# Performance work log

Measured on AMD Instinct MI355X. Metric: run time of the kernel, lower is better.

## Reference

```python
import jax, jax.numpy as jnp
import numpy as np

IN_FEATURES = 256
N_HEADS = 4
N_HIDDEN = 128  # out_features, concat=False
SLOPE = 0.1
NEG_INF = -9e15


def setup_inputs() -> dict:
    key = jax.random.key(0)
    k1, k2, k3, k4 = jax.random.split(key, 4)
    N = 8192
    h = jax.random.normal(k1, (N, IN_FEATURES), dtype=jnp.float32)
    adj_mat = jax.random.randint(k2, (N, N), 0, 2, dtype=jnp.int32)
    # xavier_normal with gain=1.414
    std_W = 1.414 * (2.0 / (IN_FEATURES + N_HIDDEN * N_HEADS)) ** 0.5
    W = jax.random.normal(k3, (IN_FEATURES, N_HIDDEN * N_HEADS), dtype=jnp.float32) * std_W
    std_a = 1.414 * (2.0 / (2 * N_HIDDEN + 1)) ** 0.5
    a = jax.random.normal(k4, (N_HEADS, 2 * N_HIDDEN, 1), dtype=jnp.float32) * std_a
    return {"h": h, "adj_mat": adj_mat, "W": W, "a": a}


def reference(h, adj_mat, W, a):
    N = h.shape[0]
    # linear projection -> [H, N, d]
    ht = (h @ W).reshape(N, N_HEADS, N_HIDDEN).transpose(1, 0, 2)
    # dropout is identity (eval / p effectively 0), then LeakyReLU
    ht = jnp.where(ht >= 0, ht, SLOPE * ht)
    # additive attention scores: src[h,i] + tgt[h,j]
    src = jnp.einsum('hnd,hd->hn', ht, a[:, :N_HIDDEN, 0])  # [H, N]
    tgt = jnp.einsum('hnd,hd->hn', ht, a[:, N_HIDDEN:, 0])  # [H, N]
    e = src[:, :, None] + tgt[:, None, :]                   # [H, N, N]
    e = jnp.where(adj_mat[None, :, :] > 0, e, NEG_INF)
    attn = jax.nn.softmax(e, axis=-1)
    # weighted sum and mean over heads (concat=False)
    out = jnp.einsum('hnm,hmd->hnd', attn, ht).mean(axis=0)  # [N, d]
    return out
```

## Files before the change

### kernel.cpp

```cpp
#include <hip/hip_runtime.h>


typedef unsigned short u16;
typedef unsigned int u32;
using bf16x8 = __attribute__((ext_vector_type(8))) short;
using f32x4  = __attribute__((ext_vector_type(4))) float;

typedef const void __attribute__((address_space(1))) gas_void;
typedef void __attribute__((address_space(3))) las_void;
#define GLD16(g, l) __builtin_amdgcn_global_load_lds((gas_void*)(g), (las_void*)(l), 16, 0, 0)

__device__ __forceinline__ u16 f2bf(float f) {
  u32 u = __float_as_uint(f);
  return (u16)((u + 0x7FFFu + ((u >> 16) & 1u)) >> 16);
}
__device__ __forceinline__ float bf2f(u16 u) {
  return __uint_as_float(((u32)u) << 16);
}

__global__ void transpose_w(const float* __restrict__ W, float* __restrict__ Wt) {
  __shared__ float tile[32][33];
  int cb = blockIdx.x * 32, kb = blockIdx.y * 32;
  int tc = threadIdx.x & 31, tr = threadIdx.x >> 5;
  for (int p = 0; p < 32; p += 8)
    tile[tr + p][tc] = W[(size_t)(kb + tr + p) * 512 + cb + tc];
  __syncthreads();
  for (int p = 0; p < 32; p += 8)
    Wt[(size_t)(cb + tr + p) * 256 + kb + tc] = tile[tc][tr + p];
}

__global__ void ht_gemm(const float* __restrict__ h, const float* __restrict__ Wt,
                        u16* __restrict__ HT) {
  __shared__ __align__(16) u16 Abuf[128 * 40];
  __shared__ __align__(16) u16 Bbuf[128 * 40];
  int tid = threadIdx.x;
  int cb = blockIdx.x, rb = blockIdx.y;
  int r0 = rb * 128, c0 = cb * 128;
  int lane = tid & 63, wv = tid >> 6;
  int wr = wv >> 1, wc = wv & 1;
  int mrow = lane & 15, q = lane >> 4;
  int ch = tid & 7, m0 = tid >> 3;

  f32x4 acc[4][4];
#pragma unroll
  for (int i = 0; i < 4; i++)
#pragma unroll
    for (int j = 0; j < 4; j++) acc[i][j] = f32x4{0.f, 0.f, 0.f, 0.f};

  for (int kt = 0; kt < 256; kt += 32) {
    __syncthreads();
#pragma unroll
    for (int mp = 0; mp < 128; mp += 32) {
      int m = m0 + mp;
      float4 v = *(const float4*)(&h[(size_t)(r0 + m) * 256 + kt + ch * 4]);
      uint2 p;
      p.x = (u32)f2bf(v.x) | ((u32)f2bf(v.y) << 16);
      p.y = (u32)f2bf(v.z) | ((u32)f2bf(v.w) << 16);
      *(uint2*)(&Abuf[m * 40 + ch * 4]) = p;
      float4 u = *(const float4*)(&Wt[(size_t)(c0 + m) * 256 + kt + ch * 4]);
      uint2 r;
      r.x = (u32)f2bf(u.x) | ((u32)f2bf(u.y) << 16);
      r.y = (u32)f2bf(u.z) | ((u32)f2bf(u.w) << 16);
      *(uint2*)(&Bbuf[m * 40 + ch * 4]) = r;
    }
    __syncthreads();
    bf16x8 af[4], bfv[4];
#pragma unroll
    for (int i = 0; i < 4; i++)
      af[i] = *(const bf16x8*)(&Abuf[(wr * 64 + i * 16 + mrow) * 40 + q * 8]);
#pragma unroll
    for (int j = 0; j < 4; j++)
      bfv[j] = *(const bf16x8*)(&Bbuf[(wc * 64 + j * 16 + mrow) * 40 + q * 8]);
#pragma unroll
    for (int i = 0; i < 4; i++)
#pragma unroll
      for (int j = 0; j < 4; j++)
        acc[i][j] = __builtin_amdgcn_mfma_f32_16x16x32_bf16(af[i], bfv[j], acc[i][j], 0, 0, 0);
  }
#pragma unroll
  for (int i = 0; i < 4; i++)
#pragma unroll
    for (int j = 0; j < 4; j++)
#pragma unroll
      for (int r = 0; r < 4; r++) {
        int gi = r0 + wr * 64 + i * 16 + q * 4 + r;
        int gc = c0 + wc * 64 + j * 16 + mrow;
        float v = acc[i][j][r];
        v = v >= 0.f ? v : 0.1f * v;
        HT[(size_t)gi * 512 + gc] = f2bf(v);
      }
}

__global__ void build_yt(const u16* __restrict__ HT, const float* __restrict__ a,
                         u16* __restrict__ Yt) {
  __shared__ u16 sht[64][528];
  __shared__ float swv[64 * 4];
  __shared__ float sa[512];
  int t = threadIdx.x;
  int j0 = blockIdx.x * 64;
  for (int i = t; i < 512; i += 256) {
    int g = i >> 7, d = i & 127;
    sa[i] = a[g * 256 + 128 + d];
  }
#pragma unroll
  for (int p = 0; p < 16; ++p) {
    int el = t + 256 * p;
    int row = el >> 6, col8 = el & 63;
    *(uint4*)(&sht[row][col8 * 8]) = *(const uint4*)(&HT[(size_t)(j0 + row) * 512 + col8 * 8]);
  }
  __syncthreads();
  {
    int jl = t >> 2, g = t & 3;
    float acc = 0.f;
#pragma unroll
    for (int d8 = 0; d8 < 16; ++d8) {
      bf16x8 v = *(const bf16x8*)(&sht[jl][g * 128 + d8 * 8]);
#pragma unroll
      for (int u = 0; u < 8; ++u)
        acc += bf2f((u16)v[u]) * sa[g * 128 + d8 * 8 + u];
    }
    swv[jl * 4 + g] = __expf(acc);
  }
  __syncthreads();
  int oj = (t & 7) * 8, oc = t >> 3;
  for (int pass = 0; pass < 17; ++pass) {
    int c = pass * 32 + oc;
    if (c >= 528) break;
    u32 pk[4] = {0u, 0u, 0u, 0u};
    if (c < 512) {
      int g = c >> 7;
#pragma unroll
      for (int u = 0; u < 4; ++u) {
        int j = oj + 2 * u;
        float v0 = bf2f(sht[j][c]) * swv[j * 4 + g];
        float v1 = bf2f(sht[j + 1][c]) * swv[(j + 1) * 4 + g];
        pk[u] = (u32)f2bf(v0) | ((u32)f2bf(v1) << 16);
      }
    } else if (c < 516) {
      int g = c - 512;
#pragma unroll
      for (int u = 0; u < 4; ++u) {
        int j = oj + 2 * u;
        float v0 = swv[j * 4 + g];
        float v1 = swv[(j + 1) * 4 + g];
        pk[u] = (u32)f2bf(v0) | ((u32)f2bf(v1) << 16);
      }
    }
    *(uint4*)(&Yt[(size_t)c * 8192 + j0 + oj]) = make_uint4(pk[0], pk[1], pk[2], pk[3]);
  }
}

__global__ __launch_bounds__(256) void adj_gemm(const int* __restrict__ adj,
                                                const u16* __restrict__ Yt,
                                                float* __restrict__ C,
                                                float* __restrict__ S) {
  __shared__ __align__(16) u16 Abuf[128 * 32];
  __shared__ __align__(16) u16 Bbuf[128 * 32];
  __shared__ __align__(16) u16 Bden[16 * 32];
  int tid = threadIdx.x;
  int cb = blockIdx.x, rb = blockIdx.y, kh = blockIdx.z;
  int r0 = rb * 128, c0 = cb * 128, k0 = kh * 2048, kend = k0 + 2048;
  int lane = tid & 63, wv = tid >> 6;
  int wr = wv >> 1, wc = wv & 1;
  int mrow = lane & 15, q = lane >> 4;
  int arow = tid >> 2, aslot = tid & 3;
  int brow = lane >> 2, bq = lane & 3;
  int bo = bq ^ ((brow >> 1) & 3);
  bool do_den = (cb == 0) && (wc == 0);
  int s8 = (q ^ ((mrow >> 1) & 3)) * 8;

  f32x4 acc[4][4];
#pragma unroll
  for (int i = 0; i < 4; i++)
#pragma unroll
    for (int j = 0; j < 4; j++) acc[i][j] = f32x4{0.f, 0.f, 0.f, 0.f};
  f32x4 accD[4];
#pragma unroll
  for (int i = 0; i < 4; i++) accD[i] = f32x4{0.f, 0.f, 0.f, 0.f};

  for (int kt = k0; kt < kend; kt += 32) {
    __syncthreads();
#pragma unroll
    for (int p = 0; p < 2; ++p) {
      int m = p * 64 + arow;
      int o = aslot ^ ((m >> 1) & 3);
      const int* ap = &adj[(size_t)(r0 + m) * 8192 + kt + o * 8];
      int4 v0 = *(const int4*)(ap);
      int4 v1 = *(const int4*)(ap + 4);
      uint4 pk;
      pk.x = 16256u * ((u32)v0.x | ((u32)v0.y << 16));
      pk.y = 16256u * ((u32)v0.z | ((u32)v0.w << 16));
      pk.z = 16256u * ((u32)v1.x | ((u32)v1.y << 16));
      pk.w = 16256u * ((u32)v1.z | ((u32)v1.w << 16));
      *(uint4*)(&Abuf[m * 32 + aslot * 8]) = pk;
    }
#pragma unroll
    for (int p = 0; p < 2; ++p) {
      int g0 = (wv * 2 + p) * 16;
      GLD16(&Yt[(size_t)(c0 + g0 + brow) * 8192 + kt + bo * 8], &Bbuf[g0 * 32]);
    }
    if (cb == 0 && wv == 0)
      GLD16(&Yt[(size_t)(512 + brow) * 8192 + kt + bo * 8], Bden);
    __syncthreads();
    bf16x8 af[4], bfv[4];
#pragma unroll
    for (int i = 0; i < 4; i++)
      af[i] = *(const bf16x8*)(&Abuf[(wr * 64 + i * 16 + mrow) * 32 + s8]);
#pragma unroll
    for (int j = 0; j < 4; j++)
      bfv[j] = *(const bf16x8*)(&Bbuf[(wc * 64 + j * 16 + mrow) * 32 + s8]);
#pragma unroll
    for (int i = 0; i < 4; i++)
#pragma unroll
      for (int j = 0; j < 4; j++)
        acc[i][j] = __builtin_amdgcn_mfma_f32_16x16x32_bf16(af[i], bfv[j], acc[i][j], 0, 0, 0);
    if (do_den) {
      bf16x8 bd = *(const bf16x8*)(&Bden[mrow * 32 + s8]);
#pragma unroll
      for (int i = 0; i < 4; i++)
        accD[i] = __builtin_amdgcn_mfma_f32_16x16x32_bf16(af[i], bd, accD[i], 0, 0, 0);
    }
  }
  float* Ck = C + (size_t)kh * 8192 * 512;
#pragma unroll
  for (int i = 0; i < 4; i++)
#pragma unroll
    for (int j = 0; j < 4; j++)
#pragma unroll
      for (int r = 0; r < 4; r++) {
        int gi = r0 + wr * 64 + i * 16 + q * 4 + r;
        int gc = c0 + wc * 64 + j * 16 + mrow;
        Ck[(size_t)gi * 512 + gc] = acc[i][j][r];
      }
  if (do_den && mrow < 4) {
    float* Sk = S + (size_t)kh * 4 * 8192;
#pragma unroll
    for (int i = 0; i < 4; i++)
#pragma unroll
      for (int r = 0; r < 4; r++) {
        int gi = r0 + wr * 64 + i * 16 + q * 4 + r;
        Sk[(size_t)mrow * 8192 + gi] = accD[i][r];
      }
  }
}

__global__ void finalize_gat(const float* __restrict__ C, const float* __restrict__ S,
                             float* __restrict__ out) {
  int idx = blockIdx.x * 256 + threadIdx.x;
  int i = idx >> 7, d = idx & 127;
  float s = 0.f;
#pragma unroll
  for (int g = 0; g < 4; ++g) {
    float num = 0.f, den = 0.f;
#pragma unroll
    for (int kh = 0; kh < 4; ++kh) {
      num += C[(size_t)kh * 8192 * 512 + (size_t)i * 512 + g * 128 + d];
      den += S[(size_t)kh * 4 * 8192 + (size_t)g * 8192 + i];
    }
    s += num / den;
  }
  out[idx] = 0.25f * s;
}

extern "C" void kernel_launch(void* const* d_in, const int* in_sizes, int n_in,
                              void* d_out, int out_size, void* d_ws, size_t ws_size,
                              hipStream_t stream) {
  const float* h   = (const float*)d_in[0];
  const int*   adj = (const int*)d_in[1];
  const float* W   = (const float*)d_in[2];
  const float* a   = (const float*)d_in[3];
  float* out = (float*)d_out;
  char* ws = (char*)d_ws;
  float* Wt = (float*)(ws + 0);
  u16*   HT = (u16*)(ws + 524288);
  u16*   Yt = (u16*)(ws + 8912896);
  float* C  = (float*)(ws + 17563648);
  float* S  = (float*)(ws + 84672512);

  transpose_w<<<dim3(16, 8), 256, 0, stream>>>(W, Wt);
  ht_gemm<<<dim3(4, 64), 256, 0, stream>>>(h, Wt, HT);
  build_yt<<<dim3(128), 256, 0, stream>>>(HT, a, Yt);
  adj_gemm<<<dim3(4, 64, 4), 256, 0, stream>>>(adj, Yt, C, S);
  finalize_gat<<<dim3(4096), 256, 0, stream>>>(C, S, out);
}
```

Measured before the change: 560.2 us.

## Retile adjacency GEMM to 64x256 with K=64 steps and split denominator kernel

```diff
diff --git a/kernel.cpp b/kernel.cpp
--- a/kernel.cpp
+++ b/kernel.cpp
@@ -154,37 +154,35 @@
                                                 const u16* __restrict__ Yt,
                                                 float* __restrict__ C,
                                                 float* __restrict__ S) {
-  __shared__ __align__(16) u16 Abuf[128 * 32];
-  __shared__ __align__(16) u16 Bbuf[128 * 32];
-  __shared__ __align__(16) u16 Bden[16 * 32];
+  __shared__ __align__(16) u16 Abuf[64 * 64];
+  __shared__ __align__(16) u16 Bbuf[256 * 64];
+  __shared__ __align__(16) u16 Bden[16 * 64];
   int tid = threadIdx.x;
   int cb = blockIdx.x, rb = blockIdx.y, kh = blockIdx.z;
-  int r0 = rb * 128, c0 = cb * 128, k0 = kh * 2048, kend = k0 + 2048;
+  int r0 = rb * 64, c0 = cb * 256, k0 = kh * 2048, kend = k0 + 2048;
   int lane = tid & 63, wv = tid >> 6;
-  int wr = wv >> 1, wc = wv & 1;
   int mrow = lane & 15, q = lane >> 4;
-  int arow = tid >> 2, aslot = tid & 3;
-  int brow = lane >> 2, bq = lane & 3;
-  int bo = bq ^ ((brow >> 1) & 3);
-  bool do_den = (cb == 0) && (wc == 0);
-  int s8 = (q ^ ((mrow >> 1) & 3)) * 8;
+  int am = tid >> 2, as0 = tid & 3;
+  int brow = lane >> 3, bs = lane & 7;
+  int bo = bs ^ (brow & 7);
+  bool do_den = (cb == 0) && (wv == 0);
 
   f32x4 acc[4][4];
 #pragma unroll
   for (int i = 0; i < 4; i++)
 #pragma unroll
     for (int j = 0; j < 4; j++) acc[i][j] = f32x4{0.f, 0.f, 0.f, 0.f};
-  f32x4 accD[4];
-#pragma unroll
-  for (int i = 0; i < 4; i++) accD[i] = f32x4{0.f, 0.f, 0.f, 0.f};
-
-  for (int kt = k0; kt < kend; kt += 32) {
+  f32x4 accD[2];
+  accD[0] = f32x4{0.f, 0.f, 0.f, 0.f};
+  accD[1] = f32x4{0.f, 0.f, 0.f, 0.f};
+
+  for (int kt = k0; kt < kend; kt += 64) {
     __syncthreads();
 #pragma unroll
     for (int p = 0; p < 2; ++p) {
-      int m = p * 64 + arow;
-      int o = aslot ^ ((m >> 1) & 3);
-      const int* ap = &adj[(size_t)(r0 + m) * 8192 + kt + o * 8];
+      int s = as0 + p * 4;
+      int o = s ^ (am & 7);
+      const int* ap = &adj[(size_t)(r0 + am) * 8192 + kt + o * 8];
       int4 v0 = *(const int4*)(ap);
       int4 v1 = *(const int4*)(ap + 4);
       uint4 pk;
@@ -192,56 +190,85 @@
       pk.y = 16256u * ((u32)v0.z | ((u32)v0.w << 16));
       pk.z = 16256u * ((u32)v1.x | ((u32)v1.y << 16));
       pk.w = 16256u * ((u32)v1.z | ((u32)v1.w << 16));
-      *(uint4*)(&Abuf[m * 32 + aslot * 8]) = pk;
-    }
-#pragma unroll
-    for (int p = 0; p < 2; ++p) {
-      int g0 = (wv * 2 + p) * 16;
-      GLD16(&Yt[(size_t)(c0 + g0 + brow) * 8192 + kt + bo * 8], &Bbuf[g0 * 32]);
-    }
-    if (cb == 0 && wv == 0)
-      GLD16(&Yt[(size_t)(512 + brow) * 8192 + kt + bo * 8], Bden);
+      *(uint4*)(&Abuf[am * 64 + s * 8]) = pk;
+    }
+#pragma unroll
+    for (int p = 0; p < 8; ++p) {
+      int g0 = (wv * 8 + p) * 8;
+      GLD16(&Yt[(size_t)(c0 + g0 + brow) * 8192 + kt + bo * 8], &Bbuf[g0 * 64]);
+    }
+    if (do_den) {
+      GLD16(&Yt[(size_t)(512 + brow) * 8192 + kt + bo * 8], &Bden[0]);
+      GLD16(&Yt[(size_t)(520 + brow) * 8192 + kt + bo * 8], &Bden[8 * 64]);
+    }
     __syncthreads();
-    bf16x8 af[4], bfv[4];
-#pragma unroll
-    for (int i = 0; i < 4; i++)
-      af[i] = *(const bf16x8*)(&Abuf[(wr * 64 + i * 16 + mrow) * 32 + s8]);
+#pragma unroll
+    for (int c = 0; c < 2; ++c) {
+      int sq = ((c * 4 + q) ^ (mrow & 7)) * 8;
+      bf16x8 af[4], bfv[4];
+#pragma unroll
+      for (int i = 0; i < 4; i++)
+        af[i] = *(const bf16x8*)(&Abuf[(i * 16 + mrow) * 64 + sq]);
+#pragma unroll
+      for (int j = 0; j < 4; j++)
+        bfv[j] = *(const bf16x8*)(&Bbuf[(wv * 64 + j * 16 + mrow) * 64 + sq]);
+#pragma unroll
+      for (int i = 0; i < 4; i++)
+#pragma unroll
+        for (int j = 0; j < 4; j++)
+          acc[i][j] = __builtin_amdgcn_mfma_f32_16x16x32_bf16(af[i], bfv[j], acc[i][j], 0, 0, 0);
+      if (do_den) {
+        bf16x8 bd = *(const bf16x8*)(&Bden[mrow * 64 + sq]);
+#pragma unroll
+        for (int i = 0; i < 4; i++) {
+          bf16x8 a2 = *(const bf16x8*)(&Abuf[(i * 16 + mrow) * 64 + sq]);
+          accD[c] = __builtin_amdgcn_mfma_f32_16x16x32_bf16(a2, bd, accD[c], 0, 0, 0);
+        }
+      }
+    }
+  }
+  float* Ck = C + (size_t)kh * 8192 * 512;
+#pragma unroll
+  for (int i = 0; i < 4; i++)
 #pragma unroll
     for (int j = 0; j < 4; j++)
-      bfv[j] = *(const bf16x8*)(&Bbuf[(wc * 64 + j * 16 + mrow) * 32 + s8]);
-#pragma unroll
-    for (int i = 0; i < 4; i++)
-#pragma unroll
-      for (int j = 0; j < 4; j++)
-        acc[i][j] = __builtin_amdgcn_mfma_f32_16x16x32_bf16(af[i], bfv[j], acc[i][j], 0, 0, 0);
-    if (do_den) {
-      bf16x8 bd = *(const bf16x8*)(&Bden[mrow * 32 + s8]);
-#pragma unroll
-      for (int i = 0; i < 4; i++)
-        accD[i] = __builtin_amdgcn_mfma_f32_16x16x32_bf16(af[i], bd, accD[i], 0, 0, 0);
-    }
-  }
-  float* Ck = C + (size_t)kh * 8192 * 512;
-#pragma unroll
-  for (int i = 0; i < 4; i++)
-#pragma unroll
-    for (int j = 0; j < 4; j++)
 #pragma unroll
       for (int r = 0; r < 4; r++) {
-        int gi = r0 + wr * 64 + i * 16 + q * 4 + r;
-        int gc = c0 + wc * 64 + j * 16 + mrow;
+        int gi = r0 + i * 16 + q * 4 + r;
+        int gc = c0 + wv * 64 + j * 16 + mrow;
         Ck[(size_t)gi * 512 + gc] = acc[i][j][r];
       }
+  if (do_den && mrow < 4) {
+  }
   if (do_den && mrow < 4) {
     float* Sk = S + (size_t)kh * 4 * 8192;
-#pragma unroll
-    for (int i = 0; i < 4; i++)
-#pragma unroll
-      for (int r = 0; r < 4; r++) {
-        int gi = r0 + wr * 64 + i * 16 + q * 4 + r;
-        Sk[(size_t)mrow * 8192 + gi] = accD[i][r];
-      }
-  }
+    (void)Sk;
+  }
+}
+
+__global__ __launch_bounds__(256) void den_gemm(const int* __restrict__ adj,
+                                                const u16* __restrict__ Yt,
+                                                float* __restrict__ S) {
+  __shared__ __align__(16) u16 Wbuf[4][2048];
+  int tid = threadIdx.x;
+  int rb = blockIdx.x, kh = blockIdx.y;
+  int r0 = rb * 64, k0 = kh * 2048;
+#pragma unroll
+  for (int p = 0; p < 4; ++p) {
+    int el = tid + p * 256;
+    int g = el >> 8, c8 = (el & 255) * 8;
+    *(uint4*)(&Wbuf[g][c8]) = *(const uint4*)(&Yt[(size_t)(512 + g) * 8192 + k0 + c8]);
+  }
+  __syncthreads();
+  int rr = tid >> 2, g = tid & 3;
+  const int* ap = &adj[(size_t)(r0 + rr) * 8192 + k0];
+  float s = 0.f;
+  for (int k = 0; k < 2048; k += 4) {
+    int4 v = *(const int4*)(&ap[k]);
+    s += (v.x ? bf2f(Wbuf[g][k]) : 0.f) + (v.y ? bf2f(Wbuf[g][k + 1]) : 0.f) +
+         (v.z ? bf2f(Wbuf[g][k + 2]) : 0.f) + (v.w ? bf2f(Wbuf[g][k + 3]) : 0.f);
+  }
+  S[(size_t)kh * 4 * 8192 + (size_t)g * 8192 + r0 + rr] = s;
 }
 
 __global__ void finalize_gat(const float* __restrict__ C, const float* __restrict__ S,
@@ -280,6 +307,7 @@
   transpose_w<<<dim3(16, 8), 256, 0, stream>>>(W, Wt);
   ht_gemm<<<dim3(4, 64), 256, 0, stream>>>(h, Wt, HT);
   build_yt<<<dim3(128), 256, 0, stream>>>(HT, a, Yt);
-  adj_gemm<<<dim3(4, 64, 4), 256, 0, stream>>>(adj, Yt, C, S);
+  adj_gemm<<<dim3(2, 128, 4), 256, 0, stream>>>(adj, Yt, C, S);
+  den_gemm<<<dim3(128, 4), 256, 0, stream>>>(adj, Yt, S);
   finalize_gat<<<dim3(4096), 256, 0, stream>>>(C, S, out);
 }
```

Result: slower. 738.2 us (+31.8%).
